# Performance work log

Hardware: AMD Instinct MI355X
Metric: run time of the kernel (lower is better)

Reference implementation:

```python
import jax, jax.numpy as jnp
import numpy as np
import math


def _instance_cl(z1, z2):
    # z1, z2: [B, T, C] -> per-element instance contrastive loss [B, T]
    B = z1.shape[0]
    z = jnp.concatenate([z1, z2], axis=0)          # [2B, T, C]
    z = z.transpose(1, 0, 2)                        # [T, 2B, C]
    sim = jnp.einsum('tic,tjc->tij', z, z)          # [T, 2B, 2B]
    # drop diagonal: tril(-1) shifted + triu(1) shifted -> [T, 2B, 2B-1]
    logits = jnp.tril(sim, -1)[:, :, :-1] + jnp.triu(sim, 1)[:, :, 1:]
    logits = -jax.nn.log_softmax(logits, axis=-1)
    i = jnp.arange(B)
    loss = (logits[:, i, B + i - 1] + logits[:, B + i, i]) / 2.0   # [T, B]
    return loss.T                                    # [B, T]


def _temporal_cl(z1, z2):
    # z1, z2: [B, T, C] -> per-timestep temporal contrastive loss [B, T]
    T = z1.shape[1]
    z = jnp.concatenate([z1, z2], axis=1)            # [B, 2T, C]
    sim = jnp.einsum('bic,bjc->bij', z, z)           # [B, 2T, 2T]
    logits = jnp.tril(sim, -1)[:, :, :-1] + jnp.triu(sim, 1)[:, :, 1:]
    logits = -jax.nn.log_softmax(logits, axis=-1)
    t = jnp.arange(T)
    return (logits[:, t, T + t - 1] + logits[:, T + t, t]) / 2.0   # [B, T]


def _contrastive_corr(z1, z2, alpha=0.5):
    # per-(batch, timestep) contrastive score, shape [B, L]
    return alpha * _instance_cl(z1, z2) + (1.0 - alpha) * _temporal_cl(z1, z2)


def setup_inputs() -> dict:
    key = jax.random.key(0)
    k1, k2, k3 = jax.random.split(key, 3)
    B, L, H, E = 4, 2048, 8, 64
    queries = jax.random.normal(k1, (B, L, H, E), dtype=jnp.float32)
    keys = jax.random.normal(k2, (B, L, H, E), dtype=jnp.float32)
    values = jax.random.normal(k3, (B, L, H, E), dtype=jnp.float32)
    attn_mask = jnp.zeros((1,), dtype=bool)  # unused; ProbMask is rebuilt internally
    return {"queries": queries, "keys": keys, "values": values, "attn_mask": attn_mask}


FACTOR = 1.0


def reference(queries, keys, values, attn_mask):
    B, L, H, E = queries.shape
    # S == L here so key/value slicing branch is a no-op
    corr = _contrastive_corr(queries.reshape(B, L, H * E),
                             keys.reshape(B, L, H * E))       # [B, L]
    top_k = int(FACTOR * math.log(L))                          # static (=7 for L=2048)
    _, index = jax.lax.top_k(corr.mean(axis=0), top_k)         # [K]
    corr_top = corr[:, index]                                  # [B, K]
    # scores[b,h,k,l] = corr_top[b,k] broadcast over h and l
    scores = jnp.broadcast_to(corr_top[:, None, :, None], (B, H, top_k, L))
    # ProbMask: mask future positions l > index[k] (causal for the selected queries)
    mask = jnp.arange(L)[None, :] > index[:, None]             # [K, L]
    scores = jnp.where(mask[None, None, :, :], -jnp.inf, scores)
    attn = jax.nn.softmax(scores, axis=-1)                     # [B, H, K, L]
    V = values.transpose(0, 2, 1, 3)                           # [B, H, L, D]
    context = jnp.cumsum(V, axis=2)                            # initial context (mask_flag=True)
    out = jnp.einsum('bhkl,bhld->bhkd', attn, V)               # [B, H, K, D]
    context = context.at[:, :, index, :].set(out)              # scatter update
    return context
```

## Files before the change

kernel.cpp:

```cpp
#include <hip/hip_runtime.h>
#include <math.h>


typedef __attribute__((ext_vector_type(8))) short short8;
typedef __attribute__((ext_vector_type(8))) unsigned short ushort8;
typedef __attribute__((ext_vector_type(4))) float f32x4;

typedef const __attribute__((address_space(1))) void* gas_ptr;
typedef __attribute__((address_space(3))) void* las_ptr;

#define EXP_OFF 80.0f

__device__ __forceinline__ void async_cp16(const void* g, void* l) {
  __builtin_amdgcn_global_load_lds((gas_ptr)g, (las_ptr)l, 16, 0, 0);
}

__device__ __forceinline__ unsigned short f2bf(float x) {
  union { float f; unsigned int u; } v; v.f = x;
  unsigned int r = v.u + 0x7FFFu + ((v.u >> 16) & 1u);
  return (unsigned short)(r >> 16);
}

__global__ __launch_bounds__(256) void convert_bf16_kernel(
    const float* __restrict__ Q, const float* __restrict__ K,
    unsigned short* __restrict__ Z) {
  int tid = blockIdx.x * 256 + threadIdx.x;
  int row = tid >> 6;
  int c0 = (tid & 63) * 8;
  int b = row >> 12, i = row & 4095;
  const float* src = (i < 2048)
      ? Q + ((size_t)(b * 2048 + i) * 512 + c0)
      : K + ((size_t)(b * 2048 + (i - 2048)) * 512 + c0);
  float4 v0 = ((const float4*)src)[0];
  float4 v1 = ((const float4*)src)[1];
  ushort8 o;
  o[0] = f2bf(v0.x); o[1] = f2bf(v0.y); o[2] = f2bf(v0.z); o[3] = f2bf(v0.w);
  o[4] = f2bf(v1.x); o[5] = f2bf(v1.y); o[6] = f2bf(v1.z); o[7] = f2bf(v1.w);
  *(ushort8*)(Z + (size_t)row * 512 + c0) = o;
}

__global__ __launch_bounds__(256, 3) void temporal_gemm_kernel(
    const unsigned short* __restrict__ Z, float* __restrict__ part) {
  int id = blockIdx.x;
  int x = id & 7;
  int b = x >> 1;
  int t = (id >> 3) * 2 + (x & 1);
  int cj = (int)((sqrtf(8.0f * (float)t + 1.0f) - 1.0f) * 0.5f);
  while ((cj + 1) * (cj + 2) / 2 <= t) cj++;
  while (cj * (cj + 1) / 2 > t) cj--;
  int ri = t - cj * (cj + 1) / 2;
  const unsigned short* Zb = Z + (size_t)b * 4096 * 512;

  __shared__ __align__(16) unsigned short As[2][128 * 32];
  __shared__ __align__(16) unsigned short Bs[2][128 * 32];

  int tid = threadIdx.x;
  int w = tid >> 6, lane = tid & 63;
  int wr = w >> 1, wc = w & 1;
  int lm = lane & 15, q = lane >> 4;
  int swz = q ^ ((lm >> 1) & 3);

  int srow = lane >> 2;
  int kq = (lane & 3) ^ ((lane >> 3) & 3);
  int rl0 = w * 16 + srow;
  int rl1 = 64 + rl0;
  const unsigned short* gA0 = Zb + (size_t)(ri * 128 + rl0) * 512 + kq * 8;
  const unsigned short* gA1 = Zb + (size_t)(ri * 128 + rl1) * 512 + kq * 8;
  const unsigned short* gB0 = Zb + (size_t)(cj * 128 + rl0) * 512 + kq * 8;
  const unsigned short* gB1 = Zb + (size_t)(cj * 128 + rl1) * 512 + kq * 8;
  int lo0 = (w * 16) * 32;
  int lo1 = (64 + w * 16) * 32;

  f32x4 acc[4][4];
#pragma unroll
  for (int mi = 0; mi < 4; mi++)
#pragma unroll
    for (int ni = 0; ni < 4; ni++) acc[mi][ni] = (f32x4)(0.f);

  async_cp16(gA0, As[0] + lo0);
  async_cp16(gA1, As[0] + lo1);
  async_cp16(gB0, Bs[0] + lo0);
  async_cp16(gB1, Bs[0] + lo1);

  for (int kc = 0; kc < 16; ++kc) {
    int cur = kc & 1;
    __syncthreads();

    if (kc < 15) {
      int go = (kc + 1) * 32;
      async_cp16(gA0 + go, As[cur ^ 1] + lo0);
      async_cp16(gA1 + go, As[cur ^ 1] + lo1);
      async_cp16(gB0 + go, Bs[cur ^ 1] + lo0);
      async_cp16(gB1 + go, Bs[cur ^ 1] + lo1);
    }

    short8 af[4], bfr[4];
#pragma unroll
    for (int mi = 0; mi < 4; mi++) {
      int ar = wr * 64 + mi * 16 + lm;
      af[mi] = *(const short8*)(As[cur] + ar * 32 + swz * 8);
    }
#pragma unroll
    for (int ni = 0; ni < 4; ni++) {
      int bc = wc * 64 + ni * 16 + lm;
      bfr[ni] = *(const short8*)(Bs[cur] + bc * 32 + swz * 8);
    }
#pragma unroll
    for (int mi = 0; mi < 4; mi++)
#pragma unroll
      for (int ni = 0; ni < 4; ni++)
        acc[mi][ni] = __builtin_amdgcn_mfma_f32_16x16x32_bf16(
            af[mi], bfr[ni], acc[mi][ni], 0, 0, 0);
  }

  float rsum[4][4];
  float csum[4];
#pragma unroll
  for (int mi = 0; mi < 4; mi++)
#pragma unroll
    for (int rr = 0; rr < 4; rr++) rsum[mi][rr] = 0.f;
#pragma unroll
  for (int ni = 0; ni < 4; ni++) csum[ni] = 0.f;

#pragma unroll
  for (int mi = 0; mi < 4; mi++) {
#pragma unroll
    for (int ni = 0; ni < 4; ni++) {
#pragma unroll
      for (int rr = 0; rr < 4; rr++) {
        int R = ri * 128 + wr * 64 + mi * 16 + q * 4 + rr;
        int Cg = cj * 128 + wc * 64 + ni * 16 + lm;
        float e = (R != Cg) ? __expf(acc[mi][ni][rr] - EXP_OFF) : 0.f;
        rsum[mi][rr] += e;
        csum[ni] += e;
      }
    }
  }

#pragma unroll
  for (int mi = 0; mi < 4; mi++) {
#pragma unroll
    for (int rr = 0; rr < 4; rr++) {
      float s = rsum[mi][rr];
      s += __shfl_xor(s, 1);
      s += __shfl_xor(s, 2);
      s += __shfl_xor(s, 4);
      s += __shfl_xor(s, 8);
      if (lm == 0) {
        int R = ri * 128 + wr * 64 + mi * 16 + q * 4 + rr;
        part[((size_t)(b * 4096 + R)) * 64 + cj * 2 + wc] = s;
      }
    }
  }

  if (ri != cj) {
#pragma unroll
    for (int ni = 0; ni < 4; ni++) {
      float s = csum[ni];
      s += __shfl_xor(s, 16);
      s += __shfl_xor(s, 32);
      if (q == 0) {
        int Cg = cj * 128 + wc * 64 + ni * 16 + lm;
        part[((size_t)(b * 4096 + Cg)) * 64 + ri * 2 + wr] = s;
      }
    }
  }
}

__global__ __launch_bounds__(256) void merge_row_kernel(
    const float* __restrict__ part, float* __restrict__ lse_temp) {
  int row = blockIdx.x * 256 + threadIdx.x;
  const float4* p = (const float4*)(part + (size_t)row * 64);
  float s = 0.f;
#pragma unroll
  for (int i = 0; i < 16; i++) {
    float4 v = p[i];
    s += v.x + v.y + v.z + v.w;
  }
  lse_temp[row] = EXP_OFF + __logf(s);
}

__global__ __launch_bounds__(256) void instance_kernel(
    const unsigned short* __restrict__ Z,
    float* __restrict__ lse_inst ,
    float* __restrict__ posdot ) {
  int wave = (blockIdx.x * 256 + threadIdx.x) >> 6;
  int t0 = wave * 2;
  int lane = threadIdx.x & 63;
  int lm = lane & 15, q = lane >> 4;
  int tt = (lm < 8) ? t0 : t0 + 1;
  int v = lm & 7;
  size_t zrow = (v < 4) ? ((size_t)v * 4096 + tt)
                        : ((size_t)(v - 4) * 4096 + 2048 + tt);
  const unsigned short* g = Z + zrow * 512 + q * 8;

  f32x4 acc0 = (f32x4)(0.f), acc1 = (f32x4)(0.f);
#pragma unroll
  for (int kc = 0; kc < 16; kc += 2) {
    short8 a0 = *(const short8*)(g + kc * 32);
    short8 a1 = *(const short8*)(g + kc * 32 + 32);
    acc0 = __builtin_amdgcn_mfma_f32_16x16x32_bf16(a0, a0, acc0, 0, 0, 0);
    acc1 = __builtin_amdgcn_mfma_f32_16x16x32_bf16(a1, a1, acc1, 0, 0, 0);
  }
  f32x4 acc = acc0 + acc1;

#pragma unroll
  for (int rr = 0; rr < 4; rr++) {
    int i = q * 4 + rr;
    float val = acc[rr];
    bool samehalf = ((i < 8) == (lm < 8));
    int t = (i < 8) ? t0 : t0 + 1;
    int iv = i & 7;
    if (samehalf && iv < 4 && (lm & 7) == iv + 4)
      posdot[iv * 2048 + t] = val;
    float dd = (samehalf && lm != i) ? val : -INFINITY;
    float mt = dd;
    mt = fmaxf(mt, __shfl_xor(mt, 1));
    mt = fmaxf(mt, __shfl_xor(mt, 2));
    mt = fmaxf(mt, __shfl_xor(mt, 4));
    float e = __expf(dd - mt);
    e += __shfl_xor(e, 1);
    e += __shfl_xor(e, 2);
    e += __shfl_xor(e, 4);
    if ((lm & 7) == 0 && samehalf) lse_inst[t * 8 + iv] = mt + __logf(e);
  }
}

__global__ __launch_bounds__(256) void combine_topk_kernel(
    const float* __restrict__ lse_inst, const float* __restrict__ lse_temp,
    const float* __restrict__ posdot, int* __restrict__ index_out) {
  __shared__ float wmax[4];
  __shared__ int widx[4];
  int tid = threadIdx.x;
  int base = tid * 8;
  float v[8];
#pragma unroll
  for (int r = 0; r < 8; r++) {
    int t = base + r;
    float sum = 0.f;
#pragma unroll
    for (int b = 0; b < 4; b++) {
      sum += 0.25f * (lse_inst[t * 8 + b] + lse_inst[t * 8 + 4 + b] +
                      lse_temp[b * 4096 + t] + lse_temp[b * 4096 + 2048 + t]) -
             posdot[b * 2048 + t];
    }
    v[r] = sum * 0.25f;
  }
  int lane = tid & 63, w = tid >> 6;
  for (int k = 0; k < 7; k++) {
    float bv = v[0];
    int bi = base;
#pragma unroll
    for (int r = 1; r < 8; r++)
      if (v[r] > bv) { bv = v[r]; bi = base + r; }
#pragma unroll
    for (int d = 1; d < 64; d <<= 1) {
      float ov = __shfl_xor(bv, d);
      int oi = __shfl_xor(bi, d);
      if (ov > bv || (ov == bv && oi < bi)) { bv = ov; bi = oi; }
    }
    if (lane == 0) { wmax[w] = bv; widx[w] = bi; }
    __syncthreads();
    float BV = wmax[0];
    int BI = widx[0];
#pragma unroll
    for (int ww = 1; ww < 4; ww++)
      if (wmax[ww] > BV || (wmax[ww] == BV && widx[ww] < BI)) {
        BV = wmax[ww];
        BI = widx[ww];
      }
    if (tid == 0) index_out[k] = BI;
    if (BI >= base && BI < base + 8) v[BI - base] = -INFINITY;
    __syncthreads();
  }
}

__global__ __launch_bounds__(1024) void cumsum_kernel(
    const float* __restrict__ V, const int* __restrict__ index,
    float* __restrict__ out) {
  int bh = blockIdx.x;
  int h = bh & 7, b = bh >> 3;
  int tid = threadIdx.x;
  int e = tid & 63, c = tid >> 6;
  __shared__ float psum[16][64];

  const float* Vbase = V + (size_t)(b * 2048) * 512 + h * 64 + e;
  float* obase = out + (size_t)bh * 2048 * 64 + e;

  int l0 = c * 128;
  float s = 0.f;
  for (int l = l0; l < l0 + 128; ++l) s += Vbase[(size_t)l * 512];
  psum[c][e] = s;

  int idx[7];
#pragma unroll
  for (int k = 0; k < 7; k++) idx[k] = index[k];
  __syncthreads();

  float run = 0.f;
#pragma unroll
  for (int cc = 0; cc < 16; ++cc) {
    float p = psum[cc][e];
    if (cc < c) run += p;
  }

  for (int l = l0; l < l0 + 128; ++l) {
    run += Vbase[(size_t)l * 512];
    float o = run;
    bool special = false;
#pragma unroll
    for (int k = 0; k < 7; k++) special = special || (idx[k] == l);
    if (special) o = run / (float)(l + 1);
    obase[(size_t)l * 64] = o;
  }
}

extern "C" void kernel_launch(void* const* d_in, const int* in_sizes, int n_in,
                              void* d_out, int out_size, void* d_ws, size_t ws_size,
                              hipStream_t stream) {
  const float* Q = (const float*)d_in[0];
  const float* K = (const float*)d_in[1];
  const float* V = (const float*)d_in[2];
  float* out = (float*)d_out;

  unsigned short* Z = (unsigned short*)d_ws;
  float* base = (float*)d_ws + 4 * 4096 * 512 / 2;
  float* part = base;
  float* lse_t = base + 4 * 4096 * 64;
  float* lse_i = lse_t + 16384;
  float* posd = lse_i + 16384;
  int* idx = (int*)(posd + 8192);

  convert_bf16_kernel<<<4096, 256, 0, stream>>>(Q, K, Z);
  temporal_gemm_kernel<<<4 * 528, 256, 0, stream>>>(Z, part);
  instance_kernel<<<256, 256, 0, stream>>>(Z, lse_i, posd);
  merge_row_kernel<<<64, 256, 0, stream>>>(part, lse_t);
  combine_topk_kernel<<<1, 256, 0, stream>>>(lse_i, lse_t, posd, idx);
  cumsum_kernel<<<32, 1024, 0, stream>>>(V, idx, out);
}
```

Measured before the change: 194.1 us.

## Split cumsum into parallel chunk-sum and scan-write kernels for more blocks

Replaces the single 32-block cumsum kernel with two kernels. The first computes per-32-row chunk partial sums across 2048 small blocks using float4 loads. The second scans with 512 blocks, each thread adding the preceding partials and then doing a 32-step serial scan. The aim is to fill the GPU's many CUs instead of 32, at the cost of an extra launch, a second read of V, and reusing the part workspace buffer for the partials.

```diff
diff --git a/kernel.cpp b/kernel.cpp
--- a/kernel.cpp
+++ b/kernel.cpp
@@ -275,36 +275,55 @@
   }
 }
 
-__global__ __launch_bounds__(1024) void cumsum_kernel(
-    const float* __restrict__ V, const int* __restrict__ index,
-    float* __restrict__ out) {
-  int bh = blockIdx.x;
+__global__ __launch_bounds__(64) void cumsum_psum_kernel(
+    const float* __restrict__ V, float* __restrict__ psum) {
+  int gb = blockIdx.x;
+  int bh = gb >> 6, g = gb & 63;
+  int h = bh & 7, b = bh >> 3;
+  int lane = threadIdx.x;
+  int ro = lane >> 4, e4 = (lane & 15) * 4;
+  const float* base =
+      V + (size_t)(b * 2048 + g * 32 + ro) * 512 + h * 64 + e4;
+  float sx = 0.f, sy = 0.f, sz = 0.f, sw = 0.f;
+#pragma unroll
+  for (int k = 0; k < 8; k++) {
+    float4 v = *(const float4*)(base + (size_t)(k * 4) * 512);
+    sx += v.x; sy += v.y; sz += v.z; sw += v.w;
+  }
+  sx += __shfl_xor(sx, 16); sy += __shfl_xor(sy, 16);
+  sz += __shfl_xor(sz, 16); sw += __shfl_xor(sw, 16);
+  sx += __shfl_xor(sx, 32); sy += __shfl_xor(sy, 32);
+  sz += __shfl_xor(sz, 32); sw += __shfl_xor(sw, 32);
+  if (ro == 0) {
+    float4 o = {sx, sy, sz, sw};
+    *(float4*)(psum + ((size_t)bh * 64 + g) * 64 + e4) = o;
+  }
+}
+
+__global__ __launch_bounds__(256) void cumsum_write_kernel(
+    const float* __restrict__ V, const float* __restrict__ psum,
+    const int* __restrict__ index, float* __restrict__ out) {
+  int blk = blockIdx.x;
+  int bh = blk >> 4, chunk = blk & 15;
   int h = bh & 7, b = bh >> 3;
   int tid = threadIdx.x;
-  int e = tid & 63, c = tid >> 6;
-  __shared__ float psum[16][64];
+  int e = tid & 63, sub = tid >> 6;
+  int g = chunk * 4 + sub;
+
+  const float* ps = psum + (size_t)bh * 64 * 64;
+  float run = 0.f;
+  for (int gg = 0; gg < g; ++gg) run += ps[gg * 64 + e];
+
+  int idx[7];
+#pragma unroll
+  for (int k = 0; k < 7; k++) idx[k] = index[k];
 
   const float* Vbase = V + (size_t)(b * 2048) * 512 + h * 64 + e;
   float* obase = out + (size_t)bh * 2048 * 64 + e;
 
-  int l0 = c * 128;
-  float s = 0.f;
-  for (int l = l0; l < l0 + 128; ++l) s += Vbase[(size_t)l * 512];
-  psum[c][e] = s;
-
-  int idx[7];
-#pragma unroll
-  for (int k = 0; k < 7; k++) idx[k] = index[k];
-  __syncthreads();
-
-  float run = 0.f;
-#pragma unroll
-  for (int cc = 0; cc < 16; ++cc) {
-    float p = psum[cc][e];
-    if (cc < c) run += p;
-  }
-
-  for (int l = l0; l < l0 + 128; ++l) {
+  int l0 = g * 32;
+#pragma unroll 4
+  for (int l = l0; l < l0 + 32; ++l) {
     run += Vbase[(size_t)l * 512];
     float o = run;
     bool special = false;
@@ -330,11 +349,13 @@
   float* lse_i = lse_t + 16384;
   float* posd = lse_i + 16384;
   int* idx = (int*)(posd + 8192);
+  float* psum = part;
 
   convert_bf16_kernel<<<4096, 256, 0, stream>>>(Q, K, Z);
   temporal_gemm_kernel<<<4 * 528, 256, 0, stream>>>(Z, part);
   instance_kernel<<<256, 256, 0, stream>>>(Z, lse_i, posd);
   merge_row_kernel<<<64, 256, 0, stream>>>(part, lse_t);
   combine_topk_kernel<<<1, 256, 0, stream>>>(lse_i, lse_t, posd, idx);
-  cumsum_kernel<<<32, 1024, 0, stream>>>(V, idx, out);
-}
+  cumsum_psum_kernel<<<2048, 64, 0, stream>>>(V, psum);
+  cumsum_write_kernel<<<512, 256, 0, stream>>>(V, psum, idx, out);
+}
```

After: 193.5 us. No clear change (-0.3%).
